# Optimization experiments

Measured on AMD Instinct MI355X. Metric: run time of the kernel, lower is better.

## Reference

```python
import jax, jax.numpy as jnp
import numpy as np

EMBED_DIM = 2048
N_HEADS = 16
HEAD_DIM = EMBED_DIM // N_HEADS


def setup_inputs() -> dict:
    key = jax.random.key(0)
    ks = jax.random.split(key, 5)
    s = 1.0 / np.sqrt(EMBED_DIM)
    x = jax.random.normal(ks[0], (2, 2048, EMBED_DIM), dtype=jnp.float32)
    W_qkv = jax.random.uniform(ks[1], (EMBED_DIM, 3 * EMBED_DIM), jnp.float32, -s, s)
    b_qkv = jax.random.uniform(ks[2], (3 * EMBED_DIM,), jnp.float32, -s, s)
    W_out = jax.random.uniform(ks[3], (EMBED_DIM, EMBED_DIM), jnp.float32, -s, s)
    b_out = jax.random.uniform(ks[4], (EMBED_DIM,), jnp.float32, -s, s)
    return {"x": x, "W_qkv": W_qkv, "b_qkv": b_qkv, "W_out": W_out, "b_out": b_out}


def reference(x, W_qkv, b_qkv, W_out, b_out):
    batch, seq_len, _ = x.shape
    qkv = jnp.einsum('bsd,de->bse', x, W_qkv) + b_qkv
    q, k, v = jnp.split(qkv, 3, axis=-1)
    # [b, h, s, hd]
    def heads(t):
        return t.reshape(batch, seq_len, N_HEADS, HEAD_DIM).transpose(0, 2, 1, 3)
    q, k, v = heads(q), heads(k), heads(v)
    scale = 1.0 / np.sqrt(HEAD_DIM)
    scores = jnp.einsum('bhqd,bhkd->bhqk', q, k) * scale  # [b,h,s,s]
    causal = jnp.tril(jnp.ones((seq_len, seq_len), dtype=bool))
    scores = jnp.where(causal, scores, -jnp.inf)
    attn = jax.nn.softmax(scores, axis=-1)
    out = jnp.einsum('bhqk,bhkd->bhqd', attn, v)
    out = out.transpose(0, 2, 1, 3).reshape(batch, seq_len, EMBED_DIM)
    return jnp.einsum('bsd,de->bse', out, W_out) + b_out
```

## Files before the change

### kernel.cpp

```cpp
#include <hip/hip_runtime.h>
#include <hip/hip_bf16.h>

#define EMBED  2048
#define SEQ    2048
#define BATCH  2
#define NHEADS 16
#define HDIM   128
#define QKVC   (3*EMBED)
#define ROWS   (BATCH*SEQ)

typedef __attribute__((ext_vector_type(8))) short bf16x8;
typedef __attribute__((ext_vector_type(4))) float f32x4;
typedef __attribute__((ext_vector_type(16))) float f32x16;

typedef const __attribute__((address_space(1))) void* gptr1_t;
typedef __attribute__((address_space(3))) void* lptr3_t;

__device__ __forceinline__ void gld16(const unsigned short* g, unsigned short* l) {
  __builtin_amdgcn_global_load_lds((gptr1_t)g, (lptr3_t)l, 16, 0, 0);
}

__device__ __forceinline__ unsigned short f2bf(float f) {
  unsigned int x = __float_as_uint(f);
  unsigned int r = (x + 0x7fffu + ((x >> 16) & 1u)) >> 16;
  return (unsigned short)r;
}

__global__ void cast_kernel(const float* __restrict__ in, unsigned short* __restrict__ out, int n4) {
  int i = blockIdx.x * 256 + threadIdx.x;
  if (i >= n4) return;
  float4 v = reinterpret_cast<const float4*>(in)[i];
  ushort4 o;
  o.x = f2bf(v.x); o.y = f2bf(v.y); o.z = f2bf(v.z); o.w = f2bf(v.w);
  reinterpret_cast<ushort4*>(out)[i] = o;
}

__global__ void transpose_cast_kernel(const float* __restrict__ in, unsigned short* __restrict__ out,
                                      int R, int C) {
  __shared__ float tile[32][33];
  int tx = threadIdx.x & 31, ty = threadIdx.x >> 5;
  int c0 = blockIdx.x * 32, r0 = blockIdx.y * 32;
  #pragma unroll
  for (int i = 0; i < 32; i += 8)
    tile[ty + i][tx] = in[(size_t)(r0 + ty + i) * C + c0 + tx];
  __syncthreads();
  #pragma unroll
  for (int i = 0; i < 32; i += 8)
    out[(size_t)(c0 + ty + i) * R + r0 + tx] = f2bf(tile[tx][ty + i]);
}

template<int MODE>
__global__ __launch_bounds__(256)
void gemm_kernel(const unsigned short* __restrict__ A,
                 const unsigned short* __restrict__ BT,
                 const float* __restrict__ bias,
                 unsigned short* __restrict__ outb,
                 unsigned short* __restrict__ vt,
                 float* __restrict__ outf,
                 int M, int N, int K) {
  __shared__ unsigned short As[2 * 128 * 32];
  __shared__ unsigned short Bs[2 * 128 * 32];
  const int t = threadIdx.x;
  const int lane = t & 63, wave = t >> 6;
  const int l31 = lane & 31, hl = lane >> 5;
  const int wm = wave >> 1, wn = wave & 1;
  const int m0 = blockIdx.y * 128, n0 = blockIdx.x * 128;

  f32x16 acc[2][2] = {};

  int aoff[2][4], boff[2][4];
  #pragma unroll
  for (int i = 0; i < 2; ++i) {
    int m = wm * 64 + i * 32 + l31;
    int pm = ((m >> 2) ^ m) & 3;
    int n = wn * 64 + i * 32 + l31;
    int pn = ((n >> 2) ^ n) & 3;
    #pragma unroll
    for (int s4 = 0; s4 < 4; ++s4) {
      int st = s4 >> 1, c = (s4 & 1) * 2 + hl;
      aoff[i][s4] = st * 4096 + (m * 4 + (c ^ pm)) * 8;
      boff[i][s4] = st * 4096 + (n * 4 + (c ^ pn)) * 8;
    }
  }
  int ldso[4];
  const unsigned short* Ag[4];
  const unsigned short* Bg[4];
  #pragma unroll
  for (int i = 0; i < 4; ++i) {
    int cc = i * 256 + t;
    int st = cc >> 9, w = cc & 511;
    int r = w >> 2, s = w & 3;
    int d = s ^ (((r >> 2) ^ r) & 3);
    ldso[i] = st * 4096 + w * 8;
    Ag[i] = A  + (size_t)(m0 + r) * K + st * 32 + d * 8;
    Bg[i] = BT + (size_t)(n0 + r) * K + st * 32 + d * 8;
  }

  for (int k0 = 0; k0 < K; k0 += 64) {
    #pragma unroll
    for (int i = 0; i < 4; ++i) gld16(Ag[i] + k0, &As[ldso[i]]);
    #pragma unroll
    for (int i = 0; i < 4; ++i) gld16(Bg[i] + k0, &Bs[ldso[i]]);
    __syncthreads();
    #pragma unroll
    for (int s4 = 0; s4 < 4; ++s4) {
      bf16x8 a0 = *(const bf16x8*)&As[aoff[0][s4]];
      bf16x8 a1 = *(const bf16x8*)&As[aoff[1][s4]];
      bf16x8 b0 = *(const bf16x8*)&Bs[boff[0][s4]];
      bf16x8 b1 = *(const bf16x8*)&Bs[boff[1][s4]];
      acc[0][0] = __builtin_amdgcn_mfma_f32_32x32x16_bf16(a0, b0, acc[0][0], 0, 0, 0);
      acc[0][1] = __builtin_amdgcn_mfma_f32_32x32x16_bf16(a0, b1, acc[0][1], 0, 0, 0);
      acc[1][0] = __builtin_amdgcn_mfma_f32_32x32x16_bf16(a1, b0, acc[1][0], 0, 0, 0);
      acc[1][1] = __builtin_amdgcn_mfma_f32_32x32x16_bf16(a1, b1, acc[1][1], 0, 0, 0);
    }
    __syncthreads();
  }

  #pragma unroll
  for (int i = 0; i < 2; ++i) {
    int rowb = m0 + wm * 64 + i * 32 + 4 * hl;
    #pragma unroll
    for (int j = 0; j < 2; ++j) {
      int col = n0 + wn * 64 + j * 32 + l31;
      float bv = bias[col];
      if (MODE == 1) {
        #pragma unroll
        for (int g = 0; g < 4; ++g)
          #pragma unroll
          for (int rr = 0; rr < 4; ++rr)
            outf[(size_t)(rowb + 8 * g + rr) * N + col] = acc[i][j][4 * g + rr] + bv;
      } else if (n0 < 2 * EMBED) {
        #pragma unroll
        for (int g = 0; g < 4; ++g)
          #pragma unroll
          for (int rr = 0; rr < 4; ++rr)
            outb[(size_t)(rowb + 8 * g + rr) * 4096 + col] = f2bf(acc[i][j][4 * g + rr] + bv);
      } else {
        int hd = col - 2 * EMBED;
        int b = rowb >> 11;
        int sbase = rowb & 2047;
        #pragma unroll
        for (int g = 0; g < 4; ++g) {
          ushort4 w;
          w.x = f2bf(acc[i][j][4 * g + 0] + bv);
          w.y = f2bf(acc[i][j][4 * g + 1] + bv);
          w.z = f2bf(acc[i][j][4 * g + 2] + bv);
          w.w = f2bf(acc[i][j][4 * g + 3] + bv);
          *(ushort4*)&vt[(((size_t)(b << 11) + hd) << 11) + sbase + 8 * g] = w;
        }
      }
    }
  }
}

__global__ __launch_bounds__(256)
void attn_kernel(const unsigned short* __restrict__ qk,
                 const unsigned short* __restrict__ vt,
                 unsigned short* __restrict__ outb) {
  __shared__ unsigned short Ks[2][64 * 128];
  __shared__ unsigned short Vs[2][64 * 128];
  __shared__ unsigned short Ps[4][16 * 72];
  const int t = threadIdx.x;
  const int lane = t & 63, wave = t >> 6;
  const int quad = lane >> 4, l16 = lane & 15;
  const int bh = blockIdx.x;
  const int pair = blockIdx.y;
  const int b = bh >> 4, h = bh & 15;
  const size_t rowbase = (size_t)b * SEQ;
  const int hq = h * HDIM;
  const unsigned short* vbase = vt + ((size_t)bh * HDIM) * SEQ;

  const float SC = 0.08838834764831845f * 1.4426950408889634f;

  #pragma unroll
  for (int half = 0; half < 2; ++half) {
    const int qt = half ? (31 - pair) : pair;
    const int qw0 = qt * 64 + wave * 16;

    bf16x8 qf[4];
    {
      const unsigned short* qrow = qk + (size_t)(rowbase + qw0 + l16) * 4096 + hq + quad * 8;
      #pragma unroll
      for (int s = 0; s < 4; ++s) qf[s] = *(const bf16x8*)(qrow + s * 32);
    }

    f32x4 o[8] = {};
    float mrow = -1e30f, lrow = 0.f;

    #pragma unroll
    for (int i = 0; i < 4; ++i) {
      int cc = i * 256 + t;
      int kv = cc >> 4, sc = cc & 15;
      int dc = sc ^ (kv & 15);
      gld16(qk + (size_t)(rowbase + kv) * 4096 + EMBED + hq + dc * 8, &Ks[0][cc * 8]);
    }
    #pragma unroll
    for (int i = 0; i < 4; ++i) {
      int cc = i * 256 + t;
      int d = cc >> 3, c = cc & 7;
      int dc = c ^ (d & 7);
      gld16(vbase + (size_t)d * SEQ + dc * 8, &Vs[0][cc * 8]);
    }

    for (int j = 0; j <= qt; ++j) {
      const int cur = j & 1;
      __syncthreads();

      if (j < qt) {
        const int kv1 = (j + 1) * 64;
        #pragma unroll
        for (int i = 0; i < 4; ++i) {
          int cc = i * 256 + t;
          int kv = cc >> 4, sc = cc & 15;
          int dc = sc ^ (kv & 15);
          gld16(qk + (size_t)(rowbase + kv1 + kv) * 4096 + EMBED + hq + dc * 8, &Ks[cur ^ 1][cc * 8]);
        }
        #pragma unroll
        for (int i = 0; i < 4; ++i) {
          int cc = i * 256 + t;
          int d = cc >> 3, c = cc & 7;
          int dc = c ^ (d & 7);
          gld16(vbase + (size_t)d * SEQ + kv1 + dc * 8, &Vs[cur ^ 1][cc * 8]);
        }
      }

      const int kv0 = j * 64;
      f32x4 sacc[4] = {};
      #pragma unroll
      for (int nb = 0; nb < 4; ++nb) {
        int kvr = nb * 16 + l16;
        #pragma unroll
        for (int ks = 0; ks < 4; ++ks) {
          int dc2 = (ks * 4 + quad) ^ (kvr & 15);
          bf16x8 kb = *(const bf16x8*)&Ks[cur][(kvr * 16 + dc2) * 8];
          sacc[nb] = __builtin_amdgcn_mfma_f32_16x16x32_bf16(kb, qf[ks], sacc[nb], 0, 0, 0);
        }
      }

      float p[4][4];
      float smax = -1e30f;
      if (j == qt) {
        const int qg = qw0 + l16;
        #pragma unroll
        for (int nb = 0; nb < 4; ++nb)
          #pragma unroll
          for (int r = 0; r < 4; ++r) {
            float v = sacc[nb][r] * SC;
            if ((kv0 + nb * 16 + quad * 4 + r) > qg) v = -1e30f;
            p[nb][r] = v;
            smax = fmaxf(smax, v);
          }
      } else {
        #pragma unroll
        for (int nb = 0; nb < 4; ++nb)
          #pragma unroll
          for (int r = 0; r < 4; ++r) {
            float v = sacc[nb][r] * SC;
            p[nb][r] = v;
            smax = fmaxf(smax, v);
          }
      }
      smax = fmaxf(smax, __shfl_xor(smax, 16));
      smax = fmaxf(smax, __shfl_xor(smax, 32));

      const float mold = mrow;
      const unsigned long long grew = __ballot(smax > mold);
      const float mnew = fmaxf(mold, smax);
      mrow = mnew;

      float rs = 0.f;
      #pragma unroll
      for (int nb = 0; nb < 4; ++nb)
        #pragma unroll
        for (int r = 0; r < 4; ++r) {
          float pv = exp2f(p[nb][r] - mnew);
          p[nb][r] = pv;
          rs += pv;
        }
      rs += __shfl_xor(rs, 16);
      rs += __shfl_xor(rs, 32);

      unsigned short* pw = &Ps[wave][0];
      #pragma unroll
      for (int nb = 0; nb < 4; ++nb) {
        __hip_bfloat162 lo = __float22bfloat162_rn(make_float2(p[nb][0], p[nb][1]));
        __hip_bfloat162 hi = __float22bfloat162_rn(make_float2(p[nb][2], p[nb][3]));
        ushort4 w;
        w.x = *(unsigned short*)&lo.x; w.y = *(unsigned short*)&lo.y;
        w.z = *(unsigned short*)&hi.x; w.w = *(unsigned short*)&hi.y;
        *(ushort4*)&pw[l16 * 72 + nb * 16 + quad * 4] = w;
      }

      if (grew) {
        float alpha = exp2f(mold - mnew);
        lrow = lrow * alpha + rs;
        #pragma unroll
        for (int r = 0; r < 4; ++r) {
          float av = __shfl(alpha, quad * 4 + r, 16);
          #pragma unroll
          for (int db = 0; db < 8; ++db) o[db][r] *= av;
        }
      } else {
        lrow += rs;
      }

      asm volatile("s_waitcnt lgkmcnt(0)" ::: "memory");
      bf16x8 pa[2];
      #pragma unroll
      for (int ks2 = 0; ks2 < 2; ++ks2)
        pa[ks2] = *(const bf16x8*)&pw[l16 * 72 + ks2 * 32 + quad * 8];

      #pragma unroll
      for (int db = 0; db < 8; ++db) {
        int d = db * 16 + l16;
        #pragma unroll
        for (int ks2 = 0; ks2 < 2; ++ks2) {
          int dc = (ks2 * 4 + quad) ^ (d & 7);
          bf16x8 vb = *(const bf16x8*)&Vs[cur][(d * 8 + dc) * 8];
          o[db] = __builtin_amdgcn_mfma_f32_16x16x32_bf16(pa[ks2], vb, o[db], 0, 0, 0);
        }
      }
    }

    #pragma unroll
    for (int r = 0; r < 4; ++r) {
      float lr = __shfl(lrow, quad * 4 + r, 16);
      float inv = 1.0f / lr;
      size_t row = rowbase + qw0 + quad * 4 + r;
      #pragma unroll
      for (int db = 0; db < 8; ++db)
        outb[row * EMBED + hq + db * 16 + l16] = f2bf(o[db][r] * inv);
    }
    __syncthreads();
  }
}

extern "C" void kernel_launch(void* const* d_in, const int* in_sizes, int n_in,
                              void* d_out, int out_size, void* d_ws, size_t ws_size,
                              hipStream_t stream) {
  const float* x    = (const float*)d_in[0];
  const float* Wqkv = (const float*)d_in[1];
  const float* bqkv = (const float*)d_in[2];
  const float* Wout = (const float*)d_in[3];
  const float* bout = (const float*)d_in[4];
  float* out = (float*)d_out;

  unsigned short* xb    = (unsigned short*)d_ws;
  unsigned short* wqkvT = xb    + (size_t)ROWS * EMBED;
  unsigned short* woutT = wqkvT + (size_t)EMBED * QKVC;
  unsigned short* qkb   = woutT + (size_t)EMBED * EMBED;
  unsigned short* vtb   = qkb   + (size_t)ROWS * 4096;
  unsigned short* attnb = vtb   + (size_t)32 * HDIM * SEQ;

  cast_kernel<<<dim3((ROWS * EMBED / 4 + 255) / 256), 256, 0, stream>>>(x, xb, ROWS * EMBED / 4);
  transpose_cast_kernel<<<dim3(QKVC / 32, EMBED / 32), 256, 0, stream>>>(Wqkv, wqkvT, EMBED, QKVC);
  transpose_cast_kernel<<<dim3(EMBED / 32, EMBED / 32), 256, 0, stream>>>(Wout, woutT, EMBED, EMBED);

  gemm_kernel<0><<<dim3(QKVC / 128, ROWS / 128), 256, 0, stream>>>(
      xb, wqkvT, bqkv, qkb, vtb, nullptr, ROWS, QKVC, EMBED);

  attn_kernel<<<dim3(32, 16), 256, 0, stream>>>(qkb, vtb, attnb);

  gemm_kernel<1><<<dim3(EMBED / 128, ROWS / 128), 256, 0, stream>>>(
      attnb, woutT, bout, nullptr, nullptr, out, ROWS, EMBED, EMBED);
}
```

Baseline: 383.2 us.

## Replace QKV projection GEMM with 256x256-tile 8-wave pipelined kernel

Adds a new GEMM kernel for the QKV projection that uses 256x256 output tiles with 512 threads, double-buffered LDS staged via global_load_lds, and XOR-swizzled LDS addressing. Loads are interleaved with MFMA quarter-steps under barriers and raised wave priority, and workgroup IDs are remapped in groups of 8 for L2 locality. Larger tiles raise arithmetic intensity and cut redundant global reads. The cost is heavy register and LDS use per block (occupancy of at most 2 blocks per CU) and only 384 blocks for a 256-CU device, which leaves a partial wave of tiles.

```diff
diff --git a/kernel.cpp b/kernel.cpp
--- a/kernel.cpp
+++ b/kernel.cpp
@@ -153,6 +153,160 @@
   }
 }
 
+#define FENCE256 asm volatile("" ::: "memory")
+#define BAR256 do { FENCE256; __builtin_amdgcn_s_barrier(); FENCE256; } while (0)
+
+#define STAGE_A256(BUF, H, KT) do { if ((KT) < NT) { \
+    gld16(Asrc[0] + (H)*128*K + (KT)*64, &As[BUF][(H)*8192 + sdst0]); \
+    gld16(Asrc[1] + (H)*128*K + (KT)*64, &As[BUF][(H)*8192 + sdst1]); } } while (0)
+#define STAGE_B256(BUF, H, KT) do { if ((KT) < NT) { \
+    gld16(Bsrc[0] + (H)*128*K + (KT)*64, &Bs[BUF][(H)*8192 + sdst0]); \
+    gld16(Bsrc[1] + (H)*128*K + (KT)*64, &Bs[BUF][(H)*8192 + sdst1]); } } while (0)
+
+#define READ_A256(BUF, MH) do { _Pragma("unroll") \
+  for (int mf = 0; mf < 4; ++mf) { \
+    av[mf][0] = *(const bf16x8*)&As[BUF][arow0 + (MH)*4096 + mf*1024 + ck0]; \
+    av[mf][1] = *(const bf16x8*)&As[BUF][arow0 + (MH)*4096 + mf*1024 + ck1]; } } while (0)
+#define READ_B256(BUF, NH, DST) do { _Pragma("unroll") \
+  for (int nf = 0; nf < 2; ++nf) { \
+    DST[nf][0] = *(const bf16x8*)&Bs[BUF][brow0 + (NH)*2048 + nf*1024 + ck0]; \
+    DST[nf][1] = *(const bf16x8*)&Bs[BUF][brow0 + (NH)*2048 + nf*1024 + ck1]; } } while (0)
+
+#define MFMA_Q256(MH, NH, B_) do { \
+  __builtin_amdgcn_s_setprio(1); \
+  _Pragma("unroll") \
+  for (int mf = 0; mf < 4; ++mf) { \
+    _Pragma("unroll") \
+    for (int nf = 0; nf < 2; ++nf) { \
+      f32x4 c = acc[(MH)*4 + mf][(NH)*2 + nf]; \
+      c = __builtin_amdgcn_mfma_f32_16x16x32_bf16(av[mf][0], B_[nf][0], c, 0, 0, 0); \
+      c = __builtin_amdgcn_mfma_f32_16x16x32_bf16(av[mf][1], B_[nf][1], c, 0, 0, 0); \
+      acc[(MH)*4 + mf][(NH)*2 + nf] = c; } } \
+  __builtin_amdgcn_s_setprio(0); } while (0)
+
+#define VMCNT256(LAST) do { \
+  if (LAST) asm volatile("s_waitcnt vmcnt(0)" ::: "memory"); \
+  else      asm volatile("s_waitcnt vmcnt(4)" ::: "memory"); } while (0)
+
+__global__ __launch_bounds__(512, 2)
+void gemm256_kernel(const unsigned short* __restrict__ A,
+                    const unsigned short* __restrict__ BT,
+                    const float* __restrict__ bias,
+                    unsigned short* __restrict__ outb,
+                    unsigned short* __restrict__ vt,
+                    int M, int N, int K) {
+  __shared__ __align__(16) unsigned short As[2][16384];
+  __shared__ __align__(16) unsigned short Bs[2][16384];
+  const int t = threadIdx.x;
+  const int lane = t & 63, wave = t >> 6;
+  const int l16 = lane & 15, quad = (lane >> 4) & 3;
+  const int wm = wave >> 2, wn = wave & 3;
+
+  const int nwg = (int)gridDim.x;
+  int swz = (int)blockIdx.x;
+  if ((nwg & 7) == 0) swz = (swz & 7) * (nwg >> 3) + (swz >> 3);
+  const int ntiles = N >> 8;
+  const int mt = swz / ntiles, nt = swz % ntiles;
+  const int m0 = mt << 8, n0 = nt << 8;
+
+  const int NT = K >> 6;
+  const int NI = NT >> 1;
+
+  f32x4 acc[8][4] = {};
+  bf16x8 av[4][2], bv0[2][2], bv1[2][2];
+
+  const unsigned short* Asrc[2];
+  const unsigned short* Bsrc[2];
+  int sdst0, sdst1;
+  {
+    int cc0 = t, cc1 = 512 + t;
+    int r0 = cc0 >> 3, c0 = cc0 & 7;
+    int r1 = cc1 >> 3, c1 = cc1 & 7;
+    Asrc[0] = A  + (size_t)(m0 + r0) * K + ((c0 ^ (r0 & 7)) << 3);
+    Asrc[1] = A  + (size_t)(m0 + r1) * K + ((c1 ^ (r1 & 7)) << 3);
+    Bsrc[0] = BT + (size_t)(n0 + r0) * K + ((c0 ^ (r0 & 7)) << 3);
+    Bsrc[1] = BT + (size_t)(n0 + r1) * K + ((c1 ^ (r1 & 7)) << 3);
+    sdst0 = cc0 << 3;
+    sdst1 = cc1 << 3;
+  }
+
+  const int ck0 = ((quad) ^ (l16 & 7)) << 3;
+  const int ck1 = ((4 + quad) ^ (l16 & 7)) << 3;
+  const int arow0 = (wm * 128 + l16) * 64;
+  const int brow0 = (wn * 64 + l16) * 64;
+
+  STAGE_A256(0, 0, 0); STAGE_A256(0, 1, 0);
+  STAGE_B256(0, 0, 0); STAGE_B256(0, 1, 0);
+  STAGE_B256(1, 0, 1); STAGE_B256(1, 1, 1);
+  asm volatile("s_waitcnt vmcnt(4)" ::: "memory");
+  BAR256;
+
+  for (int it = 0; it < NI; ++it) {
+    const int kt1 = 2 * it + 1, ktA = 2 * it + 2, ktB = 2 * it + 3;
+    const bool last = (it == NI - 1);
+
+    READ_A256(0, 0); READ_B256(0, 0, bv0);
+    STAGE_A256(1, 0, kt1);
+    BAR256; MFMA_Q256(0, 0, bv0); BAR256;
+    READ_B256(0, 1, bv1);
+    STAGE_A256(1, 1, kt1);
+    BAR256; MFMA_Q256(0, 1, bv1); BAR256;
+    READ_A256(0, 1);
+    STAGE_B256(0, 0, ktA);
+    BAR256; MFMA_Q256(1, 1, bv1); BAR256;
+    STAGE_B256(0, 1, ktA);
+    BAR256; MFMA_Q256(1, 0, bv0);
+    VMCNT256(last);
+    BAR256;
+    READ_A256(1, 0); READ_B256(1, 0, bv0);
+    STAGE_A256(0, 0, ktA);
+    BAR256; MFMA_Q256(0, 0, bv0); BAR256;
+    READ_B256(1, 1, bv1);
+    STAGE_A256(0, 1, ktA);
+    BAR256; MFMA_Q256(0, 1, bv1); BAR256;
+    READ_A256(1, 1);
+    STAGE_B256(1, 0, ktB);
+    BAR256; MFMA_Q256(1, 1, bv1); BAR256;
+    STAGE_B256(1, 1, ktB);
+    BAR256; MFMA_Q256(1, 0, bv0);
+    VMCNT256(last);
+    BAR256;
+  }
+
+  if (n0 < 2 * EMBED) {
+    #pragma unroll
+    for (int mf = 0; mf < 8; ++mf) {
+      const int row = m0 + wm * 128 + (mf >> 2) * 64 + (mf & 3) * 16 + quad * 4;
+      #pragma unroll
+      for (int nf = 0; nf < 4; ++nf) {
+        const int col = n0 + wn * 64 + (nf >> 1) * 32 + (nf & 1) * 16 + l16;
+        const float bv = bias[col];
+        #pragma unroll
+        for (int r = 0; r < 4; ++r)
+          outb[(size_t)(row + r) * 4096 + col] = f2bf(acc[mf][nf][r] + bv);
+      }
+    }
+  } else {
+    #pragma unroll
+    for (int mf = 0; mf < 8; ++mf) {
+      const int rowb = m0 + wm * 128 + (mf >> 2) * 64 + (mf & 3) * 16 + quad * 4;
+      const int b = rowb >> 11, s = rowb & 2047;
+      #pragma unroll
+      for (int nf = 0; nf < 4; ++nf) {
+        const int col = n0 + wn * 64 + (nf >> 1) * 32 + (nf & 1) * 16 + l16;
+        const int hd = col - 2 * EMBED;
+        const float bv = bias[col];
+        ushort4 w;
+        w.x = f2bf(acc[mf][nf][0] + bv);
+        w.y = f2bf(acc[mf][nf][1] + bv);
+        w.z = f2bf(acc[mf][nf][2] + bv);
+        w.w = f2bf(acc[mf][nf][3] + bv);
+        *(ushort4*)&vt[(((size_t)(b << 11) + hd) << 11) + s] = w;
+      }
+    }
+  }
+}
+
 __global__ __launch_bounds__(256)
 void attn_kernel(const unsigned short* __restrict__ qk,
                  const unsigned short* __restrict__ vt,
@@ -356,8 +510,8 @@
   transpose_cast_kernel<<<dim3(QKVC / 32, EMBED / 32), 256, 0, stream>>>(Wqkv, wqkvT, EMBED, QKVC);
   transpose_cast_kernel<<<dim3(EMBED / 32, EMBED / 32), 256, 0, stream>>>(Wout, woutT, EMBED, EMBED);
 
-  gemm_kernel<0><<<dim3(QKVC / 128, ROWS / 128), 256, 0, stream>>>(
-      xb, wqkvT, bqkv, qkb, vtb, nullptr, ROWS, QKVC, EMBED);
+  gemm256_kernel<<<dim3((QKVC / 256) * (ROWS / 256)), 512, 0, stream>>>(
+      xb, wqkvT, bqkv, qkb, vtb, ROWS, QKVC, EMBED);
 
   attn_kernel<<<dim3(32, 16), 256, 0, stream>>>(qkb, vtb, attnb);
 
```

Result: slower. 391.5 us (+2.2%).
